# Kernel tuning notes

Hardware: AMD Instinct MI355X
Metric: run time of the kernel (lower is better)

The kernel has to match this reference:

```python
import jax, jax.numpy as jnp
import numpy as np

MAX_SPAN_LENGTH = 4


def setup_inputs() -> dict:
    key = jax.random.key(0)
    ks = jax.random.split(key, 6)
    B, S, H, E = 8, 2048, 768, 32
    hidden_states = jax.random.normal(ks[0], (B, S, H), jnp.float32)
    topic_vector = jax.random.normal(ks[1], (B, H), jnp.float32)
    text_mask = jnp.ones((B, S), dtype=bool)
    length_embedding = jax.random.normal(ks[2], (MAX_SPAN_LENGTH + 1, E), jnp.float32) * 0.02
    W1 = jax.random.normal(ks[3], (3 * H + E, H), jnp.float32) * 0.02
    b1 = jnp.zeros((H,), jnp.float32)
    W2 = jax.random.normal(ks[4], (H, 1), jnp.float32) * 0.02
    b2 = jnp.zeros((1,), jnp.float32)
    return {"hidden_states": hidden_states, "topic_vector": topic_vector,
            "text_mask": text_mask, "length_embedding": length_embedding,
            "W1": W1, "b1": b1, "W2": W2, "b2": b2}


def reference(hidden_states, topic_vector, text_mask, length_embedding, W1, b1, W2, b2):
    B, S, H = hidden_states.shape
    L = MAX_SPAN_LENGTH
    NEG = jnp.float32(-jnp.inf)

    # Static span grid (text_mask is full): span k = (start, start+off), off in [0, L)
    offs = jnp.arange(L)
    starts = jnp.repeat(jnp.arange(S), L)          # [N] with N = S*L
    ends = starts + jnp.tile(offs, S)              # [N]
    valid = ends < S                               # pad spans running off the end
    ends_c = jnp.minimum(ends, S - 1)
    lengths = jnp.tile(offs + 1, S)                # [N] in [1, L]

    start_v = hidden_states[:, starts, :]          # [B,N,H] gather span starts
    end_v = hidden_states[:, ends_c, :]            # [B,N,H] gather span ends
    len_v = length_embedding[lengths]              # [N,E]
    N = starts.shape[0]
    topic = jnp.broadcast_to(topic_vector[:, None, :], (B, N, H))
    feats = jnp.concatenate(
        [topic, start_v, end_v, jnp.broadcast_to(len_v[None], (B, N, len_v.shape[-1]))],
        axis=-1)                                   # [B,N,3H+E]

    h = jax.nn.gelu(feats @ W1 + b1, approximate=False)   # [B,N,H]
    span_scores = (h @ W2)[..., 0] + b2[0]                 # [B,N]
    span_scores = jnp.where(valid[None, :], span_scores, NEG)

    # Project span scores back to tokens via masked max over covering spans
    tok = jnp.arange(S)
    cover = (tok[None, :] >= starts[:, None]) & (tok[None, :] <= ends_c[:, None])  # [N,S]
    token_scores = jnp.max(
        jnp.where(cover[None, :, :], span_scores[:, :, None], NEG), axis=1)       # [B,S]
    token_scores = jnp.where(text_mask, token_scores, NEG)
    return token_scores, span_scores
```

## Files before the change

kernel.cpp:

```cpp
#include <hip/hip_runtime.h>
#include <math.h>

#define B 8
#define S 2048
#define H 768
#define E 32
#define L 4
#define M (B*S)
#define NCOL (2*H)
#define K 768

#define NEG_SENTINEL (-1.0e30f)

typedef float v4f __attribute__((ext_vector_type(4)));
typedef short v8s __attribute__((ext_vector_type(8)));
typedef _Float16 v8h __attribute__((ext_vector_type(8)));
typedef _Float16 v4h __attribute__((ext_vector_type(4)));

__device__ __forceinline__ int cperm_true(int cp) {
  return (cp & ~63) | (((cp & 3) << 4) | ((cp >> 2) & 15));
}

__device__ __forceinline__ void bfsplit(float f, unsigned short& h, unsigned short& l) {
  unsigned u = __float_as_uint(f);
  unsigned r = u + 0x7FFF + ((u >> 16) & 1);
  h = (unsigned short)(r >> 16);
  float fh = __uint_as_float(r & 0xFFFF0000u);
  float fl = f - fh;
  unsigned u2 = __float_as_uint(fl);
  unsigned r2 = u2 + 0x7FFF + ((u2 >> 16) & 1);
  l = (unsigned short)(r2 >> 16);
}
__device__ __forceinline__ void split4(float4 f, uint2& h, uint2& l) {
  unsigned short h0,h1,h2,h3,l0,l1,l2,l3;
  bfsplit(f.x,h0,l0); bfsplit(f.y,h1,l1); bfsplit(f.z,h2,l2); bfsplit(f.w,h3,l3);
  h.x = (unsigned)h0 | ((unsigned)h1 << 16); h.y = (unsigned)h2 | ((unsigned)h3 << 16);
  l.x = (unsigned)l0 | ((unsigned)l1 << 16); l.y = (unsigned)l2 | ((unsigned)l3 << 16);
}

__device__ __forceinline__ float gelu_f(float x) {
  float y  = x * 0.70710678118654752f;
  float ay = fabsf(y);
  float t  = __builtin_amdgcn_rcpf(fmaf(0.3275911f, ay, 1.0f));
  float poly = t * fmaf(t, fmaf(t, fmaf(t, fmaf(t, 1.061405429f, -1.453152027f),
                                        1.421413741f), -0.284496736f), 0.254829592f);
  float e  = __expf(-y * y);
  float er = 1.0f - poly * e;
  er = __builtin_copysignf(er, y);
  return 0.5f * x * (1.0f + er);
}


#define SPLITA_BLOCKS 6144
#define CONVW_BLOCKS 288
#define MISC_BLOCKS 39
#define TOPICW_BLOCKS 768

__global__ __launch_bounds__(256) void prep(
    const float* __restrict__ A, const float* __restrict__ W1,
    const float* __restrict__ lenemb, const float* __restrict__ b1,
    const float* __restrict__ W2,
    _Float16* __restrict__ Af, _Float16* __restrict__ Wf,
    float* __restrict__ topicW, float* __restrict__ lenbase,
    float* __restrict__ W2p)
{
  __shared__ float t[64][65];
  int bx = blockIdx.x;
  if (bx < SPLITA_BLOCKS) {
    int c = bx * 256 + threadIdx.x;
    int mr = c & 15;
    int cell = c >> 4;
    int kc = cell % 96;
    int m16 = cell / 96;
    int m = m16 * 16 + mr;
    int k0 = kc * 8;
    float4 f0 = *(const float4*)(A + (size_t)m * K + k0);
    float4 f1 = *(const float4*)(A + (size_t)m * K + k0 + 4);
    v8h hv;
    hv[0] = (_Float16)f0.x; hv[1] = (_Float16)f0.y;
    hv[2] = (_Float16)f0.z; hv[3] = (_Float16)f0.w;
    hv[4] = (_Float16)f1.x; hv[5] = (_Float16)f1.y;
    hv[6] = (_Float16)f1.z; hv[7] = (_Float16)f1.w;
    *(v8h*)(Af + (size_t)c * 8) = hv;
  } else if (bx < SPLITA_BLOCKS + CONVW_BLOCKS) {
    int blk = bx - SPLITA_BLOCKS;
    int kb = blk % (K / 64);
    int nb = blk / (K / 64);
    int k0 = kb * 64, n0 = nb * 64;
    int tn = threadIdx.x & 63, tk = threadIdx.x >> 6;
    int n = n0 + tn;
    const float* src = (n < H) ? (W1 + (size_t)(H + k0) * H + n)
                               : (W1 + (size_t)(2 * H + k0) * H + (n - H));
    #pragma unroll
    for (int s = 0; s < 16; s++) {
      int kk = tk + s * 4;
      t[kk][tn] = src[(size_t)kk * H];
    }
    __syncthreads();
    int tkk = threadIdx.x & 63, tnn = threadIdx.x >> 6;
    #pragma unroll
    for (int s = 0; s < 16; s++) {
      int nn = tnn + s * 4;
      float v = t[tkk][nn];
      int n_g = n0 + nn;
      int kk_g = k0 + tkk;
      size_t go = ((size_t)((n_g >> 4) * 96 + (kk_g >> 3)) * 16 + (n_g & 15)) * 8
                + (kk_g & 7);
      Wf[go] = (_Float16)v;
    }
  } else {
    int idx = (bx - SPLITA_BLOCKS - CONVW_BLOCKS) * 256 + threadIdx.x;
    if (idx < L * H) {
      int l = idx / H, cp = idx % H;
      int h = cperm_true(cp);
      float s = b1[h];
      const float* le = lenemb + (size_t)(l + 1) * E;
      #pragma unroll
      for (int e = 0; e < E; e++)
        s = fmaf(le[e], W1[(size_t)(3 * H + e) * H + h], s);
      lenbase[idx] = s;
    } else if (idx < L * H + B * H) {
      topicW[idx - L * H] = 0.f;
    } else if (idx < L * H + B * H + H) {
      int cp = idx - L * H - B * H;
      W2p[cp] = W2[cperm_true(cp)];
    }
  }
}

__global__ __launch_bounds__(256, 2) void gemm_mfma(
    const _Float16* __restrict__ Af, const _Float16* __restrict__ Wf,
    const float* __restrict__ topic, const float* __restrict__ W1,
    float* __restrict__ topicW,
    _Float16* __restrict__ P, _Float16* __restrict__ Q)
{
  __shared__ float red[4][64];
  int tid = threadIdx.x, lane = tid & 63, wv = tid >> 6;
  int f = blockIdx.x;

  if (f >= (M / 128) * (NCOL / 128)) {
    int tw = f - (M / 128) * (NCOL / 128);
    int b = tw / 96;
    int r = tw % 96;
    int h0 = (r / 8) * 64;
    int kc0 = (r % 8) * 96;
    int hcol = tid & 63, ksub = tid >> 6;
    const float* tp = topic + (size_t)b * H;
    float s = 0.f;
    #pragma unroll
    for (int i = 0; i < 24; i++) {
      int k = kc0 + ksub * 24 + i;
      s = fmaf(tp[k], W1[(size_t)k * H + h0 + hcol], s);
    }
    red[ksub][hcol] = s;
    __syncthreads();
    if (tid < 64) {
      int cpo = ((tid & 15) << 2) | (tid >> 4);
      float tot = red[0][tid] + red[1][tid] + red[2][tid] + red[3][tid];
      atomicAdd(&topicW[(size_t)b * H + h0 + cpo], tot);
    }
    return;
  }

  int xcd = f & 7, g = f >> 3;
  int mb = xcd * 16 + (g / 12);
  int nb = g % 12;
  int wm = (wv >> 1) * 64, wn = (wv & 1) * 64;
  int kg = lane >> 4, fr = lane & 15;

  int aoff[4], boff[4];
  #pragma unroll
  for (int i = 0; i < 4; i++) {
    aoff[i] = ((mb * 8 + (wm >> 4) + i) * 96) * 128 + lane * 8;
    boff[i] = ((nb * 8 + (wn >> 4) + i) * 96) * 128 + lane * 8;
  }

  v4f acc[4][4];
  #pragma unroll
  for (int i = 0; i < 4; i++)
    #pragma unroll
    for (int j = 0; j < 4; j++) { v4f z = {0.f,0.f,0.f,0.f}; acc[i][j] = z; }

  v8h a[3][4], b[3][4];

  #define LOADF(BUF, IT)                                                       \
    { int ko = (IT) * 512;                                                     \
      _Pragma("unroll")                                                        \
      for (int i = 0; i < 4; i++) {                                            \
        a[BUF][i] = *(const v8h*)(Af + aoff[i] + ko);                          \
        b[BUF][i] = *(const v8h*)(Wf + boff[i] + ko);                          \
      } }

  #define COMPUTE(BUF)                                                         \
    { __builtin_amdgcn_s_setprio(1);                                           \
      _Pragma("unroll")                                                        \
      for (int j = 0; j < 4; j++)                                              \
        _Pragma("unroll")                                                      \
        for (int i = 0; i < 4; i++)                                            \
          acc[i][j] = __builtin_amdgcn_mfma_f32_16x16x32_f16(                  \
              a[BUF][i], b[BUF][j], acc[i][j], 0, 0, 0);                       \
      __builtin_amdgcn_s_setprio(0); }

  LOADF(0, 0);
  LOADF(1, 1);
  #pragma unroll
  for (int o = 0; o < 8; o++) {
    int i2 = (3 * o + 2) % 24;
    int i3 = (3 * o + 3) % 24;
    int i4 = (3 * o + 4) % 24;
    LOADF(2, i2);
    COMPUTE(0);
    LOADF(0, i3);
    COMPUTE(1);
    LOADF(1, i4);
    COMPUTE(2);
  }
  #undef LOADF
  #undef COMPUTE

  int m0 = mb * 128, n0 = nb * 128;
  _Float16* outB = (nb < 6) ? P : Q;
  int cb = (nb < 6) ? n0 : (n0 - H);
  int cbase = cb + wn + fr * 4;
  #pragma unroll
  for (int i = 0; i < 4; i++) {
    int row0 = m0 + wm + i * 16 + kg * 4;
    #pragma unroll
    for (int r = 0; r < 4; r++) {
      v4h pk;
      pk[0] = (_Float16)acc[i][0][r];
      pk[1] = (_Float16)acc[i][1][r];
      pk[2] = (_Float16)acc[i][2][r];
      pk[3] = (_Float16)acc[i][3][r];
      *(v4h*)(outB + (size_t)(row0 + r) * H + cbase) = pk;
    }
  }
}


__global__ __launch_bounds__(256) void combine(
    const _Float16* __restrict__ P, const _Float16* __restrict__ Q,
    const float* __restrict__ topicW, const float* __restrict__ lenbase,
    const float* __restrict__ W2p, const float* __restrict__ b2,
    float* __restrict__ spanOut)
{
  int tid = threadIdx.x, lane = tid & 63, wv = tid >> 6;
  int siteBase = blockIdx.x * 16;
  int b = siteBase >> 11;
  int gs0 = siteBase + wv * 4;
  int s0 = gs0 & (S - 1);
  int gmax = (b + 1) * S - 1;
  int c0 = 4 * lane;
  float bb2 = b2[0];

  float acc[4][4];
  #pragma unroll
  for (int si = 0; si < 4; si++)
    #pragma unroll
    for (int l = 0; l < L; l++) acc[si][l] = 0.f;

  #pragma unroll
  for (int j = 0; j < 3; j++) {
    int co = c0 + 256 * j;
    float4 w2 = *(const float4*)(W2p + co);
    float4 tv = *(const float4*)(topicW + (size_t)b * H + co);
    float4 bv[4];
    #pragma unroll
    for (int l = 0; l < L; l++) {
      float4 lv = *(const float4*)(lenbase + (size_t)l * H + co);
      bv[l].x = tv.x + lv.x; bv[l].y = tv.y + lv.y;
      bv[l].z = tv.z + lv.z; bv[l].w = tv.w + lv.w;
    }
    float4 p[4], q[7];
    #pragma unroll
    for (int si = 0; si < 4; si++) {
      v4h ph = *(const v4h*)(P + (size_t)(gs0 + si) * H + co);
      p[si].x = (float)ph[0]; p[si].y = (float)ph[1];
      p[si].z = (float)ph[2]; p[si].w = (float)ph[3];
    }
    #pragma unroll
    for (int r = 0; r < 7; r++) {
      int grow = gs0 + r; if (grow > gmax) grow = gmax;
      v4h qh = *(const v4h*)(Q + (size_t)grow * H + co);
      q[r].x = (float)qh[0]; q[r].y = (float)qh[1];
      q[r].z = (float)qh[2]; q[r].w = (float)qh[3];
    }
    #pragma unroll
    for (int si = 0; si < 4; si++) {
      #pragma unroll
      for (int l = 0; l < L; l++) {
        int r = si + l;
        float a0 = acc[si][l];
        a0 = fmaf(gelu_f(bv[l].x + p[si].x + q[r].x), w2.x, a0);
        a0 = fmaf(gelu_f(bv[l].y + p[si].y + q[r].y), w2.y, a0);
        a0 = fmaf(gelu_f(bv[l].z + p[si].z + q[r].z), w2.z, a0);
        a0 = fmaf(gelu_f(bv[l].w + p[si].w + q[r].w), w2.w, a0);
        acc[si][l] = a0;
      }
    }
  }

  #pragma unroll
  for (int off = 32; off; off >>= 1)
    #pragma unroll
    for (int si = 0; si < 4; si++)
      #pragma unroll
      for (int l = 0; l < L; l++)
        acc[si][l] += __shfl_xor(acc[si][l], off, 64);

  if (lane == 0) {
    #pragma unroll
    for (int si = 0; si < 4; si++) {
      int s = s0 + si;
      #pragma unroll
      for (int l = 0; l < L; l++) {
        float v = (s + l < S) ? (acc[si][l] + bb2) : NEG_SENTINEL;
        spanOut[(size_t)b * (S * L) + (size_t)s * L + l] = v;
      }
    }
  }
}

__global__ void token_max(const float* __restrict__ spanOut,
                          float* __restrict__ tokenOut)
{
  int idx = blockIdx.x * 256 + threadIdx.x;
  if (idx >= B * S) return;
  int b = idx >> 11, t = idx & (S - 1);
  float m = -INFINITY;
  int slo = max(t - (L - 1), 0);
  for (int sb = slo; sb <= t; sb++)
    for (int l = t - sb; l < L; l++)
      m = fmaxf(m, spanOut[(size_t)b * (S * L) + sb * L + l]);
  tokenOut[idx] = m;
}


__global__ __launch_bounds__(256) void conv_w_old(
    const float* __restrict__ W1,
    unsigned short* __restrict__ Wh, unsigned short* __restrict__ Wl)
{
  __shared__ float t[64][65];
  int kb = blockIdx.x % (K / 64);
  int nb = blockIdx.x / (K / 64);
  int k0 = kb * 64, n0 = nb * 64;
  int tn = threadIdx.x & 63, tk = threadIdx.x >> 6;
  int n = n0 + tn;
  const float* src = (n < H) ? (W1 + (size_t)(H + k0) * H + n)
                             : (W1 + (size_t)(2 * H + k0) * H + (n - H));
  #pragma unroll
  for (int s = 0; s < 16; s++) {
    int kk = tk + s * 4;
    t[kk][tn] = src[(size_t)kk * H];
  }
  __syncthreads();
  int tkk = threadIdx.x & 63, tnn = threadIdx.x >> 6;
  #pragma unroll
  for (int s = 0; s < 16; s++) {
    int nn = tnn + s * 4;
    float v = t[tkk][nn];
    unsigned short hi, lo;
    bfsplit(v, hi, lo);
    size_t go = (size_t)(n0 + nn) * K + k0 + tkk;
    Wh[go] = hi; Wl[go] = lo;
  }
}

__global__ __launch_bounds__(256) void gemm_old(
    const float* __restrict__ A,
    const unsigned short* __restrict__ Wh,
    const unsigned short* __restrict__ Wl,
    float* __restrict__ P, float* __restrict__ Q)
{
  __shared__ __align__(16) unsigned short Ah_t[128 * 32];
  __shared__ __align__(16) unsigned short Al_t[128 * 32];
  __shared__ __align__(16) unsigned short Bh_t[128 * 32];
  __shared__ __align__(16) unsigned short Bl_t[128 * 32];

  int tid = threadIdx.x;
  int lane = tid & 63, wv = tid >> 6;
  int n0 = blockIdx.x * 128;
  int m0 = blockIdx.y * 128;
  int sr = tid >> 1;
  int sc = (tid & 1) * 16;
  const float* Ap = A + (size_t)(m0 + sr) * K + sc;
  const unsigned short* Bph = Wh + (size_t)(n0 + sr) * K + sc;
  const unsigned short* Bpl = Wl + (size_t)(n0 + sr) * K + sc;
  int wm = (wv >> 1) * 64;
  int wn = (wv & 1) * 64;
  int kg = lane >> 4;
  int fr = lane & 15;

  v4f acc[4][4];
  #pragma unroll
  for (int i = 0; i < 4; i++)
    #pragma unroll
    for (int j = 0; j < 4; j++) { v4f z = {0.f,0.f,0.f,0.f}; acc[i][j] = z; }

  for (int k0 = 0; k0 < K; k0 += 32) {
    float4 a0 = *(const float4*)(Ap + k0);
    float4 a1 = *(const float4*)(Ap + k0 + 4);
    float4 a2 = *(const float4*)(Ap + k0 + 8);
    float4 a3 = *(const float4*)(Ap + k0 + 12);
    uint4 bh0 = *(const uint4*)(Bph + k0);
    uint4 bh1 = *(const uint4*)(Bph + k0 + 8);
    uint4 bl0 = *(const uint4*)(Bpl + k0);
    uint4 bl1 = *(const uint4*)(Bpl + k0 + 8);
    __syncthreads();
    uint2 h0,h1,h2,h3, l0,l1,l2,l3;
    split4(a0,h0,l0); split4(a1,h1,l1); split4(a2,h2,l2); split4(a3,h3,l3);
    uint4 H0 = {h0.x,h0.y,h1.x,h1.y}, H1 = {h2.x,h2.y,h3.x,h3.y};
    uint4 L0 = {l0.x,l0.y,l1.x,l1.y}, L1 = {l2.x,l2.y,l3.x,l3.y};
    *(uint4*)&Ah_t[sr*32 + sc]     = H0;
    *(uint4*)&Ah_t[sr*32 + sc + 8] = H1;
    *(uint4*)&Al_t[sr*32 + sc]     = L0;
    *(uint4*)&Al_t[sr*32 + sc + 8] = L1;
    *(uint4*)&Bh_t[sr*32 + sc]     = bh0;
    *(uint4*)&Bh_t[sr*32 + sc + 8] = bh1;
    *(uint4*)&Bl_t[sr*32 + sc]     = bl0;
    *(uint4*)&Bl_t[sr*32 + sc + 8] = bl1;
    __syncthreads();
    v8s ah[4], al[4], bh[4], bl[4];
    #pragma unroll
    for (int i = 0; i < 4; i++) {
      ah[i] = *(v8s*)&Ah_t[(wm + i*16 + fr)*32 + kg*8];
      al[i] = *(v8s*)&Al_t[(wm + i*16 + fr)*32 + kg*8];
      bh[i] = *(v8s*)&Bh_t[(wn + i*16 + fr)*32 + kg*8];
      bl[i] = *(v8s*)&Bl_t[(wn + i*16 + fr)*32 + kg*8];
    }
    #pragma unroll
    for (int i = 0; i < 4; i++)
      #pragma unroll
      for (int j = 0; j < 4; j++) {
        acc[i][j] = __builtin_amdgcn_mfma_f32_16x16x32_bf16(ah[i], bh[j], acc[i][j], 0, 0, 0);
        acc[i][j] = __builtin_amdgcn_mfma_f32_16x16x32_bf16(ah[i], bl[j], acc[i][j], 0, 0, 0);
        acc[i][j] = __builtin_amdgcn_mfma_f32_16x16x32_bf16(al[i], bh[j], acc[i][j], 0, 0, 0);
      }
  }
  float* outB = (n0 < H) ? P : Q;
  int cb = (n0 < H) ? n0 : (n0 - H);
  #pragma unroll
  for (int i = 0; i < 4; i++) {
    int row0 = m0 + wm + i*16 + kg*4;
    #pragma unroll
    for (int j = 0; j < 4; j++) {
      int col = cb + wn + j*16 + fr;
      #pragma unroll
      for (int r = 0; r < 4; r++)
        outB[(size_t)(row0 + r) * H + col] = acc[i][j][r];
    }
  }
}

__global__ void compute_base(const float* __restrict__ topic,
                             const float* __restrict__ lenemb,
                             const float* __restrict__ W1,
                             const float* __restrict__ b1,
                             float* __restrict__ base)
{
  int idx = blockIdx.x * 256 + threadIdx.x;
  if (idx >= B * L * H) return;
  int h = idx % H;
  int bl = idx / H;
  int l = bl % L;
  int b = bl / L;
  float sacc = b1[h];
  const float* t = topic + b * H;
  for (int k = 0; k < H; k++)
    sacc = fmaf(t[k], W1[(size_t)k * H + h], sacc);
  const float* le = lenemb + (l + 1) * E;
  for (int e = 0; e < E; e++)
    sacc = fmaf(le[e], W1[(size_t)(3 * H + e) * H + h], sacc);
  base[idx] = sacc;
}

__global__ __launch_bounds__(256) void combine_f32(
    const float* __restrict__ P, const float* __restrict__ Q,
    const float* __restrict__ base,
    const float* __restrict__ W2, const float* __restrict__ b2,
    float* __restrict__ spanOut)
{
  int tid = threadIdx.x, lane = tid & 63, wv = tid >> 6;
  int siteBase = blockIdx.x * 16;
  int b = siteBase >> 11;
  int c0 = 4 * lane;
  float4 w2v[3], bv[4][3];
  #pragma unroll
  for (int j = 0; j < 3; j++) {
    w2v[j] = *(const float4*)(W2 + c0 + 256 * j);
    #pragma unroll
    for (int l = 0; l < L; l++)
      bv[l][j] = *(const float4*)(base + ((size_t)(b * L + l)) * H + c0 + 256 * j);
  }
  float bb2 = b2[0];

  #pragma unroll
  for (int si = 0; si < 4; si++) {
    int site = siteBase + wv * 4 + si;
    int s = site & (S - 1);
    const float* Prow = P + (size_t)site * H;
    float4 p[3];
    #pragma unroll
    for (int j = 0; j < 3; j++) p[j] = *(const float4*)(Prow + c0 + 256 * j);
    float acc[4];
    #pragma unroll
    for (int l = 0; l < L; l++) {
      int e = min(s + l, S - 1);
      const float* Qrow = Q + ((size_t)(b * S + e)) * H;
      float a = 0.f;
      #pragma unroll
      for (int j = 0; j < 3; j++) {
        float4 q = *(const float4*)(Qrow + c0 + 256 * j);
        a = fmaf(gelu_f(bv[l][j].x + p[j].x + q.x), w2v[j].x, a);
        a = fmaf(gelu_f(bv[l][j].y + p[j].y + q.y), w2v[j].y, a);
        a = fmaf(gelu_f(bv[l][j].z + p[j].z + q.z), w2v[j].z, a);
        a = fmaf(gelu_f(bv[l][j].w + p[j].w + q.w), w2v[j].w, a);
      }
      acc[l] = a;
    }
    #pragma unroll
    for (int off = 32; off; off >>= 1)
      #pragma unroll
      for (int l = 0; l < L; l++) acc[l] += __shfl_xor(acc[l], off, 64);
    if (lane == 0) {
      #pragma unroll
      for (int l = 0; l < L; l++) {
        float v = (s + l < S) ? (acc[l] + bb2) : NEG_SENTINEL;
        spanOut[(size_t)b * (S * L) + s * L + l] = v;
      }
    }
  }
}

extern "C" void kernel_launch(void* const* d_in, const int* in_sizes, int n_in,
                              void* d_out, int out_size, void* d_ws, size_t ws_size,
                              hipStream_t stream) {
  const float* hidden = (const float*)d_in[0];
  const float* topic  = (const float*)d_in[1];
  const float* lenemb = (const float*)d_in[3];
  const float* W1     = (const float*)d_in[4];
  const float* b1     = (const float*)d_in[5];
  const float* W2     = (const float*)d_in[6];
  const float* b2     = (const float*)d_in[7];

  float* out = (float*)d_out;
  float* tokenOut = out;
  float* spanOut  = out + B * S;

  size_t need = (size_t)(2 * M * H + M * K + NCOL * K) * 2
              + (size_t)(B * H + L * H + H) * 4;

  if (ws_size >= need) {
    _Float16* Pm = (_Float16*)d_ws;
    _Float16* Qm = Pm + (size_t)M * H;
    _Float16* Af = Qm + (size_t)M * H;
    _Float16* Wf = Af + (size_t)M * K;
    float* topicW  = (float*)(Wf + (size_t)NCOL * K);
    float* lenbase = topicW + (size_t)B * H;
    float* W2p     = lenbase + (size_t)L * H;

    prep<<<SPLITA_BLOCKS + CONVW_BLOCKS + MISC_BLOCKS, 256, 0, stream>>>(
        hidden, W1, lenemb, b1, W2, Af, Wf, topicW, lenbase, W2p);
    gemm_mfma<<<(M / 128) * (NCOL / 128) + TOPICW_BLOCKS, 256, 0, stream>>>(
        Af, Wf, topic, W1, topicW, Pm, Qm);
    combine<<<(B * S) / 16, 256, 0, stream>>>(Pm, Qm, topicW, lenbase, W2p, b2, spanOut);
    token_max<<<(B * S + 255) / 256, 256, 0, stream>>>(spanOut, tokenOut);
  } else {
    float* Pm = (float*)d_ws;
    float* Qm = Pm + (size_t)M * H;
    unsigned short* Wh = (unsigned short*)(Qm + (size_t)M * H);
    unsigned short* Wl = Wh + (size_t)NCOL * K;
    float* base = (float*)(Wl + (size_t)NCOL * K);

    conv_w_old<<<(K / 64) * (NCOL / 64), 256, 0, stream>>>(W1, Wh, Wl);
    compute_base<<<(B * L * H + 255) / 256, 256, 0, stream>>>(topic, lenemb, W1, b1, base);
    gemm_old<<<dim3(NCOL / 128, M / 128), 256, 0, stream>>>(hidden, Wh, Wl, Pm, Qm);
    combine_f32<<<(B * S) / 16, 256, 0, stream>>>(Pm, Qm, base, W2, b2, spanOut);
    token_max<<<(B * S + 255) / 256, 256, 0, stream>>>(spanOut, tokenOut);
  }
}
```

Baseline: 177.2 us.

## Stage GEMM tiles through LDS with direct global-to-LDS loads and double buffering

The GEMM main loop no longer loads A/W fragments straight from global memory into registers. It streams each K-step tile into a 64KB double-buffered LDS region using global_load_lds, then reads the fragments from LDS, so global loads are shared and coalesced within a block. The prep A-conversion is also restructured: each block converts 16 rows through LDS to write the tiled f16 layout with contiguous stores, using fewer blocks. The trade-offs are a __syncthreads per K-step, high LDS use that limits occupancy, and dropping the min-2-blocks launch bound.

```diff
diff --git a/kernel.cpp b/kernel.cpp
--- a/kernel.cpp
+++ b/kernel.cpp
@@ -51,7 +51,7 @@
 }
 
 
-#define SPLITA_BLOCKS 6144
+#define SPLITA_BLOCKS 1024
 #define CONVW_BLOCKS 288
 #define MISC_BLOCKS 39
 #define TOPICW_BLOCKS 768
@@ -64,25 +64,33 @@
     float* __restrict__ topicW, float* __restrict__ lenbase,
     float* __restrict__ W2p)
 {
-  __shared__ float t[64][65];
+  __shared__ __align__(16) char pshm[16 * 776 * 2];
   int bx = blockIdx.x;
   if (bx < SPLITA_BLOCKS) {
-    int c = bx * 256 + threadIdx.x;
-    int mr = c & 15;
-    int cell = c >> 4;
-    int kc = cell % 96;
-    int m16 = cell / 96;
-    int m = m16 * 16 + mr;
-    int k0 = kc * 8;
-    float4 f0 = *(const float4*)(A + (size_t)m * K + k0);
-    float4 f1 = *(const float4*)(A + (size_t)m * K + k0 + 4);
-    v8h hv;
-    hv[0] = (_Float16)f0.x; hv[1] = (_Float16)f0.y;
-    hv[2] = (_Float16)f0.z; hv[3] = (_Float16)f0.w;
-    hv[4] = (_Float16)f1.x; hv[5] = (_Float16)f1.y;
-    hv[6] = (_Float16)f1.z; hv[7] = (_Float16)f1.w;
-    *(v8h*)(Af + (size_t)c * 8) = hv;
+    _Float16* sl = (_Float16*)pshm;
+    const float4* Ab = (const float4*)(A + (size_t)bx * 16 * K);
+    #pragma unroll
+    for (int rnd = 0; rnd < 12; rnd++) {
+      int o4 = rnd * 256 + threadIdx.x;
+      float4 fv = Ab[o4];
+      int r = o4 / 192;
+      int c = (o4 - r * 192) * 4;
+      v4h hv;
+      hv[0] = (_Float16)fv.x; hv[1] = (_Float16)fv.y;
+      hv[2] = (_Float16)fv.z; hv[3] = (_Float16)fv.w;
+      *(v4h*)(&sl[r * 776 + c]) = hv;
+    }
+    __syncthreads();
+    _Float16* dst = Af + (size_t)bx * 12288;
+    #pragma unroll
+    for (int rnd = 0; rnd < 6; rnd++) {
+      int cc = rnd * 256 + threadIdx.x;
+      int r = cc & 15, kc = cc >> 4;
+      v8h hv = *(v8h*)(&sl[r * 776 + kc * 8]);
+      *(v8h*)(dst + (size_t)cc * 8) = hv;
+    }
   } else if (bx < SPLITA_BLOCKS + CONVW_BLOCKS) {
+    float (*t)[65] = (float(*)[65])pshm;
     int blk = bx - SPLITA_BLOCKS;
     int kb = blk % (K / 64);
     int nb = blk / (K / 64);
@@ -128,17 +136,18 @@
   }
 }
 
-__global__ __launch_bounds__(256, 2) void gemm_mfma(
+__global__ __launch_bounds__(256) void gemm_mfma(
     const _Float16* __restrict__ Af, const _Float16* __restrict__ Wf,
     const float* __restrict__ topic, const float* __restrict__ W1,
     float* __restrict__ topicW,
     _Float16* __restrict__ P, _Float16* __restrict__ Q)
 {
-  __shared__ float red[4][64];
+  __shared__ __align__(16) char smem[65536];
   int tid = threadIdx.x, lane = tid & 63, wv = tid >> 6;
   int f = blockIdx.x;
 
   if (f >= (M / 128) * (NCOL / 128)) {
+    float (*red)[64] = (float(*)[64])smem;
     int tw = f - (M / 128) * (NCOL / 128);
     int b = tw / 96;
     int r = tw % 96;
@@ -165,14 +174,19 @@
   int xcd = f & 7, g = f >> 3;
   int mb = xcd * 16 + (g / 12);
   int nb = g % 12;
-  int wm = (wv >> 1) * 64, wn = (wv & 1) * 64;
+  int wm2 = wv >> 1, wn2 = wv & 1;
   int kg = lane >> 4, fr = lane & 15;
 
-  int aoff[4], boff[4];
-  #pragma unroll
-  for (int i = 0; i < 4; i++) {
-    aoff[i] = ((mb * 8 + (wm >> 4) + i) * 96) * 128 + lane * 8;
-    boff[i] = ((nb * 8 + (wn >> 4) + i) * 96) * 128 + lane * 8;
+  const _Float16* gsrc[8];
+  #pragma unroll
+  for (int p = 0; p < 8; p++) {
+    int pi = wv * 8 + p;
+    int isB = pi >> 4;
+    int q = pi & 15;
+    int rc16 = q >> 1, j = q & 1;
+    const _Float16* base = isB ? Wf : Af;
+    int rowblk = isB ? (nb * 8 + rc16) : (mb * 8 + rc16);
+    gsrc[p] = base + ((size_t)rowblk * 96 + (size_t)j * 4) * 128 + lane * 8;
   }
 
   v4f acc[4][4];
@@ -181,50 +195,57 @@
     #pragma unroll
     for (int j = 0; j < 4; j++) { v4f z = {0.f,0.f,0.f,0.f}; acc[i][j] = z; }
 
-  v8h a[3][4], b[3][4];
-
-  #define LOADF(BUF, IT)                                                       \
-    { int ko = (IT) * 512;                                                     \
+  #define STAGE(CUR, T)                                                        \
+    { char* lb = smem + (CUR) * 32768;                                         \
+      size_t ko = (size_t)(T) * 1024;                                          \
       _Pragma("unroll")                                                        \
-      for (int i = 0; i < 4; i++) {                                            \
-        a[BUF][i] = *(const v8h*)(Af + aoff[i] + ko);                          \
-        b[BUF][i] = *(const v8h*)(Wf + boff[i] + ko);                          \
-      } }
-
-  #define COMPUTE(BUF)                                                         \
-    { __builtin_amdgcn_s_setprio(1);                                           \
+      for (int p = 0; p < 8; p++)                                              \
+        __builtin_amdgcn_global_load_lds(                                      \
+            (const __attribute__((address_space(1))) unsigned int*)(gsrc[p] + ko), \
+            (__attribute__((address_space(3))) unsigned int*)(lb + (wv * 8 + p) * 1024), \
+            16, 0, 0); }
+
+  #define COMPUTE(CUR)                                                         \
+    { char* lb = smem + (CUR) * 32768;                                         \
+      v8h a_[2][4], b_[2][4];                                                  \
       _Pragma("unroll")                                                        \
-      for (int j = 0; j < 4; j++)                                              \
+      for (int j = 0; j < 2; j++)                                              \
         _Pragma("unroll")                                                      \
-        for (int i = 0; i < 4; i++)                                            \
-          acc[i][j] = __builtin_amdgcn_mfma_f32_16x16x32_f16(                  \
-              a[BUF][i], b[BUF][j], acc[i][j], 0, 0, 0);                       \
+        for (int i = 0; i < 4; i++) {                                          \
+          a_[j][i] = *(const v8h*)(lb + ((wm2 * 4 + i) * 2 + j) * 1024 + lane * 16); \
+          b_[j][i] = *(const v8h*)(lb + 16384 + ((wn2 * 4 + i) * 2 + j) * 1024 + lane * 16); \
+        }                                                                      \
+      __builtin_amdgcn_s_setprio(1);                                           \
+      _Pragma("unroll")                                                        \
+      for (int j = 0; j < 2; j++)                                              \
+        _Pragma("unroll")                                                      \
+        for (int q = 0; q < 4; q++)                                            \
+          _Pragma("unroll")                                                    \
+          for (int i = 0; i < 4; i++)                                          \
+            acc[i][q] = __builtin_amdgcn_mfma_f32_16x16x32_f16(                \
+                a_[j][i], b_[j][q], acc[i][q], 0, 0, 0);                       \
       __builtin_amdgcn_s_setprio(0); }
 
-  LOADF(0, 0);
-  LOADF(1, 1);
-  #pragma unroll
-  for (int o = 0; o < 8; o++) {
-    int i2 = (3 * o + 2) % 24;
-    int i3 = (3 * o + 3) % 24;
-    int i4 = (3 * o + 4) % 24;
-    LOADF(2, i2);
-    COMPUTE(0);
-    LOADF(0, i3);
-    COMPUTE(1);
-    LOADF(1, i4);
-    COMPUTE(2);
-  }
-  #undef LOADF
+  STAGE(0, 0);
+  __syncthreads();
+  int cur = 0;
+  for (int t = 0; t < 11; t++) {
+    STAGE(cur ^ 1, t + 1);
+    COMPUTE(cur);
+    __syncthreads();
+    cur ^= 1;
+  }
+  COMPUTE(cur);
+  #undef STAGE
   #undef COMPUTE
 
   int m0 = mb * 128, n0 = nb * 128;
   _Float16* outB = (nb < 6) ? P : Q;
   int cb = (nb < 6) ? n0 : (n0 - H);
-  int cbase = cb + wn + fr * 4;
+  int cbase = cb + wn2 * 64 + fr * 4;
   #pragma unroll
   for (int i = 0; i < 4; i++) {
-    int row0 = m0 + wm + i * 16 + kg * 4;
+    int row0 = m0 + wm2 * 64 + i * 16 + kg * 4;
     #pragma unroll
     for (int r = 0; r < 4; r++) {
       v4h pk;
```

Result: faster. 173.7 us, median of 2 (-2.0%).

## Stage A fp16 conversion through LDS and split combine columns across waves

Applied to the files above, without the earlier changes.

The prep A-conversion path now has each block load 16 full rows with coalesced float4 reads. It converts them to fp16 in LDS, then writes the 16-row interleaved layout the GEMM expects, replacing the strided per-thread gathers. The combine kernel now gives each block 4 span starts with 3 waves, each handling one 256-column slice. The per-wave partial sums are reduced through shared memory. This quadruples the number of combine blocks and removes the serial 3-iteration column loop, at the cost of an extra barrier and a cross-wave reduction.

```diff
diff --git a/kernel.cpp b/kernel.cpp
--- a/kernel.cpp
+++ b/kernel.cpp
@@ -51,7 +51,7 @@
 }
 
 
-#define SPLITA_BLOCKS 6144
+#define SPLITA_BLOCKS 1024
 #define CONVW_BLOCKS 288
 #define MISC_BLOCKS 39
 #define TOPICW_BLOCKS 768
@@ -64,25 +64,33 @@
     float* __restrict__ topicW, float* __restrict__ lenbase,
     float* __restrict__ W2p)
 {
-  __shared__ float t[64][65];
+  __shared__ __align__(16) char pshm[16 * 776 * 2];
   int bx = blockIdx.x;
   if (bx < SPLITA_BLOCKS) {
-    int c = bx * 256 + threadIdx.x;
-    int mr = c & 15;
-    int cell = c >> 4;
-    int kc = cell % 96;
-    int m16 = cell / 96;
-    int m = m16 * 16 + mr;
-    int k0 = kc * 8;
-    float4 f0 = *(const float4*)(A + (size_t)m * K + k0);
-    float4 f1 = *(const float4*)(A + (size_t)m * K + k0 + 4);
-    v8h hv;
-    hv[0] = (_Float16)f0.x; hv[1] = (_Float16)f0.y;
-    hv[2] = (_Float16)f0.z; hv[3] = (_Float16)f0.w;
-    hv[4] = (_Float16)f1.x; hv[5] = (_Float16)f1.y;
-    hv[6] = (_Float16)f1.z; hv[7] = (_Float16)f1.w;
-    *(v8h*)(Af + (size_t)c * 8) = hv;
+    _Float16* sl = (_Float16*)pshm;
+    const float4* Ab = (const float4*)(A + (size_t)bx * 16 * K);
+    #pragma unroll
+    for (int rnd = 0; rnd < 12; rnd++) {
+      int o4 = rnd * 256 + threadIdx.x;
+      float4 fv = Ab[o4];
+      int r = o4 / 192;
+      int c = (o4 - r * 192) * 4;
+      v4h hv;
+      hv[0] = (_Float16)fv.x; hv[1] = (_Float16)fv.y;
+      hv[2] = (_Float16)fv.z; hv[3] = (_Float16)fv.w;
+      *(v4h*)(&sl[r * 776 + c]) = hv;
+    }
+    __syncthreads();
+    _Float16* dst = Af + (size_t)bx * 12288;
+    #pragma unroll
+    for (int rnd = 0; rnd < 6; rnd++) {
+      int cc = rnd * 256 + threadIdx.x;
+      int r = cc & 15, kc = cc >> 4;
+      v8h hv = *(v8h*)(&sl[r * 776 + kc * 8]);
+      *(v8h*)(dst + (size_t)cc * 8) = hv;
+    }
   } else if (bx < SPLITA_BLOCKS + CONVW_BLOCKS) {
+    float (*t)[65] = (float(*)[65])pshm;
     int blk = bx - SPLITA_BLOCKS;
     int kb = blk % (K / 64);
     int nb = blk / (K / 64);
@@ -238,65 +246,56 @@
 }
 
 
-__global__ __launch_bounds__(256) void combine(
+__global__ __launch_bounds__(192) void combine(
     const _Float16* __restrict__ P, const _Float16* __restrict__ Q,
     const float* __restrict__ topicW, const float* __restrict__ lenbase,
     const float* __restrict__ W2p, const float* __restrict__ b2,
     float* __restrict__ spanOut)
 {
+  __shared__ float part[3][16];
   int tid = threadIdx.x, lane = tid & 63, wv = tid >> 6;
-  int siteBase = blockIdx.x * 16;
-  int b = siteBase >> 11;
-  int gs0 = siteBase + wv * 4;
+  int gs0 = blockIdx.x * 4;
+  int b = gs0 >> 11;
   int s0 = gs0 & (S - 1);
   int gmax = (b + 1) * S - 1;
-  int c0 = 4 * lane;
-  float bb2 = b2[0];
+  int co = 4 * lane + 256 * wv;
+
+  float4 w2 = *(const float4*)(W2p + co);
+  float4 tv = *(const float4*)(topicW + (size_t)b * H + co);
+  float4 bv[4];
+  #pragma unroll
+  for (int l = 0; l < L; l++) {
+    float4 lv = *(const float4*)(lenbase + (size_t)l * H + co);
+    bv[l].x = tv.x + lv.x; bv[l].y = tv.y + lv.y;
+    bv[l].z = tv.z + lv.z; bv[l].w = tv.w + lv.w;
+  }
+  float4 p[4], q[7];
+  #pragma unroll
+  for (int si = 0; si < 4; si++) {
+    v4h ph = *(const v4h*)(P + (size_t)(gs0 + si) * H + co);
+    p[si].x = (float)ph[0]; p[si].y = (float)ph[1];
+    p[si].z = (float)ph[2]; p[si].w = (float)ph[3];
+  }
+  #pragma unroll
+  for (int r = 0; r < 7; r++) {
+    int grow = gs0 + r; if (grow > gmax) grow = gmax;
+    v4h qh = *(const v4h*)(Q + (size_t)grow * H + co);
+    q[r].x = (float)qh[0]; q[r].y = (float)qh[1];
+    q[r].z = (float)qh[2]; q[r].w = (float)qh[3];
+  }
 
   float acc[4][4];
   #pragma unroll
-  for (int si = 0; si < 4; si++)
-    #pragma unroll
-    for (int l = 0; l < L; l++) acc[si][l] = 0.f;
-
-  #pragma unroll
-  for (int j = 0; j < 3; j++) {
-    int co = c0 + 256 * j;
-    float4 w2 = *(const float4*)(W2p + co);
-    float4 tv = *(const float4*)(topicW + (size_t)b * H + co);
-    float4 bv[4];
+  for (int si = 0; si < 4; si++) {
     #pragma unroll
     for (int l = 0; l < L; l++) {
-      float4 lv = *(const float4*)(lenbase + (size_t)l * H + co);
-      bv[l].x = tv.x + lv.x; bv[l].y = tv.y + lv.y;
-      bv[l].z = tv.z + lv.z; bv[l].w = tv.w + lv.w;
-    }
-    float4 p[4], q[7];
-    #pragma unroll
-    for (int si = 0; si < 4; si++) {
-      v4h ph = *(const v4h*)(P + (size_t)(gs0 + si) * H + co);
-      p[si].x = (float)ph[0]; p[si].y = (float)ph[1];
-      p[si].z = (float)ph[2]; p[si].w = (float)ph[3];
-    }
-    #pragma unroll
-    for (int r = 0; r < 7; r++) {
-      int grow = gs0 + r; if (grow > gmax) grow = gmax;
-      v4h qh = *(const v4h*)(Q + (size_t)grow * H + co);
-      q[r].x = (float)qh[0]; q[r].y = (float)qh[1];
-      q[r].z = (float)qh[2]; q[r].w = (float)qh[3];
-    }
-    #pragma unroll
-    for (int si = 0; si < 4; si++) {
-      #pragma unroll
-      for (int l = 0; l < L; l++) {
-        int r = si + l;
-        float a0 = acc[si][l];
-        a0 = fmaf(gelu_f(bv[l].x + p[si].x + q[r].x), w2.x, a0);
-        a0 = fmaf(gelu_f(bv[l].y + p[si].y + q[r].y), w2.y, a0);
-        a0 = fmaf(gelu_f(bv[l].z + p[si].z + q[r].z), w2.z, a0);
-        a0 = fmaf(gelu_f(bv[l].w + p[si].w + q[r].w), w2.w, a0);
-        acc[si][l] = a0;
-      }
+      int r = si + l;
+      float a0 = 0.f;
+      a0 = fmaf(gelu_f(bv[l].x + p[si].x + q[r].x), w2.x, a0);
+      a0 = fmaf(gelu_f(bv[l].y + p[si].y + q[r].y), w2.y, a0);
+      a0 = fmaf(gelu_f(bv[l].z + p[si].z + q[r].z), w2.z, a0);
+      a0 = fmaf(gelu_f(bv[l].w + p[si].w + q[r].w), w2.w, a0);
+      acc[si][l] = a0;
     }
   }
 
@@ -310,14 +309,18 @@
 
   if (lane == 0) {
     #pragma unroll
-    for (int si = 0; si < 4; si++) {
-      int s = s0 + si;
-      #pragma unroll
-      for (int l = 0; l < L; l++) {
-        float v = (s + l < S) ? (acc[si][l] + bb2) : NEG_SENTINEL;
-        spanOut[(size_t)b * (S * L) + (size_t)s * L + l] = v;
-      }
-    }
+    for (int si = 0; si < 4; si++)
+      #pragma unroll
+      for (int l = 0; l < L; l++)
+        part[wv][si * 4 + l] = acc[si][l];
+  }
+  __syncthreads();
+  if (tid < 16) {
+    int si = tid >> 2, l = tid & 3;
+    float v = part[0][tid] + part[1][tid] + part[2][tid] + b2[0];
+    int s = s0 + si;
+    if (s + l >= S) v = NEG_SENTINEL;
+    spanOut[(size_t)b * (S * L) + (size_t)s * L + l] = v;
   }
 }
 
@@ -563,7 +566,7 @@
         hidden, W1, lenemb, b1, W2, Af, Wf, topicW, lenbase, W2p);
     gemm_mfma<<<(M / 128) * (NCOL / 128) + TOPICW_BLOCKS, 256, 0, stream>>>(
         Af, Wf, topic, W1, topicW, Pm, Qm);
-    combine<<<(B * S) / 16, 256, 0, stream>>>(Pm, Qm, topicW, lenbase, W2p, b2, spanOut);
+    combine<<<M / 4, 192, 0, stream>>>(Pm, Qm, topicW, lenbase, W2p, b2, spanOut);
     token_max<<<(B * S + 255) / 256, 256, 0, stream>>>(spanOut, tokenOut);
   } else {
     float* Pm = (float*)d_ws;
```

New measurement: 177.8 us. About the same (+0.3%).
